# Kernel tuning notes

Hardware: AMD Instinct MI355X
Metric: run time of the kernel (lower is better)

## Reference

```python
import jax, jax.numpy as jnp
import numpy as np

B, L, H, HEADS, N_NODE = 1024, 200, 128, 8, 200000
MAXN = L + 1  # max_n_node
D = H // HEADS
EPS = 1e-12


def setup_inputs() -> dict:
    key = jax.random.key(0)
    ks = jax.random.split(key, 20)
    lengths = jax.random.randint(ks[0], (B,), 1, L + 1)
    mask = (jnp.arange(L)[None, :] < lengths[:, None]).astype(jnp.int32)  # contiguous 1s
    alias_inputs = jax.random.randint(ks[1], (B, L), 0, MAXN)
    items = jax.random.randint(ks[2], (B, MAXN), 0, N_NODE)

    def lin_w(k, o, i):
        return (jax.random.normal(k, (o, i), jnp.float32) * 0.1)

    inp = dict(
        alias_inputs=alias_inputs,
        items=items,
        mask=mask,
        emb_W=jax.random.normal(ks[3], (N_NODE, H), jnp.float32) * 0.1,
        # LastAttenion params
        W0=lin_w(ks[4], H, H), b0=jax.random.normal(ks[5], (H,), jnp.float32) * 0.1,
        W1=lin_w(ks[6], H, H), b1=jax.random.normal(ks[7], (H,), jnp.float32) * 0.1,
        W2=lin_w(ks[8], H, H), b2=jax.random.normal(ks[9], (H,), jnp.float32) * 0.1,
        # linear_q[0] (last_k = 1)
        Wq=lin_w(ks[10], H, H), bq=jax.random.normal(ks[11], (H,), jnp.float32) * 0.1,
        # linear_transform (2H -> H)
        Wt=lin_w(ks[12], H, 2 * H), bt=jax.random.normal(ks[13], (H,), jnp.float32) * 0.1,
        ln_g=jax.random.normal(ks[14], (H,), jnp.float32) * 0.1,
        ln_b=jax.random.normal(ks[15], (H,), jnp.float32) * 0.1,
    )
    return inp


def reference(alias_inputs, items, mask, emb_W, W0, b0, W1, b1, W2, b2, Wq, bq, Wt, bt, ln_g, ln_b):
    maskf = mask.astype(jnp.float32)
    # hidden = normalize(embedding(items)); dropout off (eval)
    hidden = emb_W[items]                                                  # [B, MAXN, H]
    hidden = hidden / (jnp.linalg.norm(hidden, axis=-1, keepdims=True) + EPS)
    # per-batch gather: seq_hidden[b, t] = hidden[b, alias_inputs[b, t]]
    seq = jnp.take_along_axis(hidden, alias_inputs[..., None], axis=1)     # [B, L, H]
    seq = seq * maskf[..., None]
    seq = seq / (jnp.linalg.norm(seq, axis=-1, keepdims=True) + EPS)
    # compute_scores
    lengths = mask.sum(1)
    last_idx = lengths - 1                                                 # >= 0 (lengths >= 1)
    ht_last = seq[jnp.arange(B), last_idx]                                 # [B, H]  (ht0 too)
    hts = (ht_last @ Wq.T + bq)[:, None, :]                                # [B, 1, H]
    # torch.norm over dim=1 (size 1) == elementwise abs
    hts = hts / (jnp.linalg.norm(hts, axis=1, keepdims=True) + EPS)
    # LastAttenion (last_k = 1, no lp-pool, eval dropout off)
    q0 = (hts @ W0.T + b0).reshape(B * HEADS, 1, D)                        # [B*h, 1, d]
    q1 = (seq @ W1.T + b1).reshape(B * HEADS, L, D)                        # [B*h, L, d]
    q2 = (seq @ W2.T + b2).reshape(B, L, HEADS, D)                         # [B, L, h, d]
    alpha = jax.nn.sigmoid(jnp.einsum('bkd,bld->bkl', q0, q1))             # [B*h, 1, L]
    alpha = alpha.reshape(B, HEADS, L).transpose(0, 2, 1)                  # [B, L, h]
    alpha = jax.nn.softmax(2.0 * alpha, axis=1)
    a = jnp.sum((alpha[..., None] * q2).reshape(B, L, H) * maskf[..., None], axis=1)  # [B, H]
    # layernorm eps=1e-8
    mu = a.mean(-1, keepdims=True)
    var = ((a - mu) ** 2).mean(-1, keepdims=True)
    a = (a - mu) / jnp.sqrt(var + 1e-8) * ln_g + ln_b
    a = jnp.concatenate([a, ht_last], axis=1) @ Wt.T + bt                  # [B, H]
    # norm=True branch
    a = a / (jnp.linalg.norm(a, axis=1, keepdims=True) + EPS)
    b = emb_W[1:]
    b = b / (jnp.linalg.norm(b, axis=1, keepdims=True) + EPS)
    return a, b.T                                                          # [B,H], [H, N_NODE-1]
```

## Files before the change

kernel.cpp:

```cpp
#include <hip/hip_runtime.h>
#include <math.h>

typedef unsigned int uint;
typedef unsigned short ushort;

__device__ __forceinline__ float b2f(ushort u){
  union { uint i; float f; } v; v.i = ((uint)u) << 16; return v.f;
}
__device__ __forceinline__ ushort f2b(float f){
  union { float f; uint i; } v; v.f = f;
  uint i = v.i;
  i += 0x7fffu + ((i >> 16) & 1u);
  return (ushort)(i >> 16);
}
__device__ __forceinline__ float wred(float v){
  #pragma unroll
  for (int s = 32; s > 0; s >>= 1) v += __shfl_xor(v, s, 64);
  return v;
}
__device__ __forceinline__ float gred16(float v){
  v += __shfl_xor(v, 1, 64);
  v += __shfl_xor(v, 2, 64);
  v += __shfl_xor(v, 4, 64);
  v += __shfl_xor(v, 8, 64);
  return v;
}
__device__ __forceinline__ float sane(float v){ return isfinite(v) ? v : 0.f; }
__device__ __forceinline__ int iclamp(int v, int lo, int hi){ return v < lo ? lo : (v > hi ? hi : v); }

__device__ __forceinline__ void gather_norm8(const void* emb, int isf, int it, int p, float x[8]){
  if (isf){
    const float4* q = (const float4*)((const float*)emb + (size_t)it * 128);
    float4 u = q[p * 2], u2 = q[p * 2 + 1];
    x[0] = u.x; x[1] = u.y; x[2] = u.z; x[3] = u.w;
    x[4] = u2.x; x[5] = u2.y; x[6] = u2.z; x[7] = u2.w;
  } else {
    uint4 u = ((const uint4*)((const ushort*)emb + (size_t)it * 128))[p];
    x[0] = b2f((ushort)u.x); x[1] = b2f((ushort)(u.x >> 16));
    x[2] = b2f((ushort)u.y); x[3] = b2f((ushort)(u.y >> 16));
    x[4] = b2f((ushort)u.z); x[5] = b2f((ushort)(u.z >> 16));
    x[6] = b2f((ushort)u.w); x[7] = b2f((ushort)(u.w >> 16));
  }
  float ss = 0.f;
  #pragma unroll
  for (int e = 0; e < 8; ++e) ss += x[e] * x[e];
  ss = gred16(ss);
  float inv = 1.f / (sqrtf(ss) + 1e-12f);
  #pragma unroll
  for (int e = 0; e < 8; ++e) x[e] *= inv;
  float ss2 = 0.f;
  #pragma unroll
  for (int e = 0; e < 8; ++e) ss2 += x[e] * x[e];
  ss2 = gred16(ss2);
  float inv2 = 1.f / (sqrtf(ss2) + 1e-12f);
  #pragma unroll
  for (int e = 0; e < 8; ++e) x[e] *= inv2;
}

#define OUTB 131072

#define C_W0T 0
#define C_W1  16384
#define C_W2T 32768
#define C_WQT 49152
#define C_WTT 65536
#define C_B0  98304
#define C_B1  98432
#define C_B2  98560
#define C_BQ  98688
#define C_BT  98816
#define C_G   98944
#define C_BB  99072
#define C_TOT 99200

__global__ __launch_bounds__(256) void k_detect(const ushort* __restrict__ emb,
                                                int* __restrict__ flag){
  __shared__ int s_bad;
  if (threadIdx.x == 0) s_bad = 0;
  __syncthreads();
  int bad = 0;
  for (int i = threadIdx.x; i < 8192; i += 256){
    float v = fabsf(b2f(emb[i]));
    if (!(v <= 1e4f)) bad = 1;
  }
  if (bad) s_bad = 1;
  __syncthreads();
  if (threadIdx.x == 0) flag[0] = s_bad;
}

__global__ __launch_bounds__(256) void k_wts(
    const void* W0, const void* b0, const void* W1, const void* b1,
    const void* W2, const void* b2, const void* Wq, const void* bq,
    const void* Wt, const void* bt, const void* g, const void* bb,
    const int* __restrict__ flag, float* __restrict__ wts){
  int j = blockIdx.x * 256 + threadIdx.x;
  if (j >= C_TOT) return;
  const int isf = flag[0];
  const void* src; int si;
  if (j < 16384)      { int k = j >> 7, h = j & 127; src = W0; si = h * 128 + k; }
  else if (j < 32768) { src = W1; si = j - 16384; }
  else if (j < 49152) { int i = j - 32768; int k = i >> 7, h = i & 127; src = W2; si = h * 128 + k; }
  else if (j < 65536) { int i = j - 49152; int k = i >> 7, h = i & 127; src = Wq; si = h * 128 + k; }
  else if (j < 98304) { int i = j - 65536; int k = i >> 7, h = i & 127; src = Wt; si = h * 256 + k; }
  else {
    int i = j - 98304; int arr = i >> 7;
    const void* tab[7] = { b0, b1, b2, bq, bt, g, bb };
    src = tab[arr]; si = i & 127;
  }
  wts[j] = isf ? ((const float*)src)[si] : b2f(((const ushort*)src)[si]);
}

__global__ __launch_bounds__(256) void k_bout(const void* __restrict__ emb,
                                              const int* __restrict__ flag,
                                              void* __restrict__ outv){
  __shared__ float tile[64 * 129];
  const int t = threadIdx.x, gid = t >> 4, p = t & 15;
  const int base = blockIdx.x * 64;
  const int isf = flag[0];
  for (int i = gid; i < 64; i += 16){
    int gi = base + i;
    if (gi < 199999){
      float x[8];
      if (isf){
        const float4* q = (const float4*)((const float*)emb + (size_t)(gi + 1) * 128);
        float4 u = q[p * 2], u2 = q[p * 2 + 1];
        x[0] = u.x; x[1] = u.y; x[2] = u.z; x[3] = u.w;
        x[4] = u2.x; x[5] = u2.y; x[6] = u2.z; x[7] = u2.w;
      } else {
        uint4 u = ((const uint4*)((const ushort*)emb + (size_t)(gi + 1) * 128))[p];
        x[0] = b2f((ushort)u.x); x[1] = b2f((ushort)(u.x >> 16));
        x[2] = b2f((ushort)u.y); x[3] = b2f((ushort)(u.y >> 16));
        x[4] = b2f((ushort)u.z); x[5] = b2f((ushort)(u.z >> 16));
        x[6] = b2f((ushort)u.w); x[7] = b2f((ushort)(u.w >> 16));
      }
      float ss = 0.f;
      #pragma unroll
      for (int e = 0; e < 8; ++e) ss += x[e] * x[e];
      ss = gred16(ss);
      float inv = 1.f / (sqrtf(ss) + 1e-12f);
      #pragma unroll
      for (int e = 0; e < 8; ++e) tile[i * 129 + p * 8 + e] = x[e] * inv;
    }
  }
  __syncthreads();
  for (int it = 0; it < 32; ++it){
    int idx = it * 256 + t;
    int h = idx >> 6, n = idx & 63;
    int gi = base + n;
    if (gi < 199999){
      float val = sane(tile[n * 129 + h]);
      if (isf) ((float*)outv)[OUTB + (size_t)h * 199999 + gi] = val;
      else     ((ushort*)outv)[OUTB + (size_t)h * 199999 + gi] = f2b(val);
    }
  }
}

__global__ __launch_bounds__(128) void k_prep(
    const int* __restrict__ alias_, const int* __restrict__ items,
    const int* __restrict__ mask, const void* __restrict__ emb,
    const float* __restrict__ wts, const int* __restrict__ flag,
    float* __restrict__ ws_ht, float* __restrict__ ws_X0,
    float* __restrict__ ws_c1, int* __restrict__ ws_len){
  __shared__ float s_ht[128], s_hts[128], s_X0s[128];
  __shared__ float s_red[8];
  __shared__ int s_item;
  const int b = blockIdx.x, t = threadIdx.x, w = t >> 6;
  const int isf = flag[0];

  int mv = mask[b * 200 + t] + (t < 72 ? mask[b * 200 + 128 + t] : 0);
  float lv = wred((float)mv);
  if ((t & 63) == 0) s_red[w] = lv;
  __syncthreads();
  int len = iclamp((int)(s_red[0] + s_red[1] + 0.5f), 1, 200);
  if (t == 0){
    ws_len[b] = len;
    int a = iclamp(alias_[b * 200 + len - 1], 0, 200);
    s_item = iclamp(items[b * 201 + a], 0, 199999);
  }
  __syncthreads();

  float v = isf ? ((const float*)emb)[(size_t)s_item * 128 + t]
                : b2f(((const ushort*)emb)[(size_t)s_item * 128 + t]);
  float ss = wred(v * v);
  if ((t & 63) == 0) s_red[2 + w] = ss;
  __syncthreads();
  v = v / (sqrtf(s_red[2] + s_red[3]) + 1e-12f);
  float ss2 = wred(v * v);
  if ((t & 63) == 0) s_red[4 + w] = ss2;
  __syncthreads();
  v = v / (sqrtf(s_red[4] + s_red[5]) + 1e-12f);
  s_ht[t] = v;
  ws_ht[b * 128 + t] = v;
  __syncthreads();

  {
    double acc = (double)wts[C_BQ + t];
    for (int k = 0; k < 128; ++k)
      acc += (double)wts[C_WQT + k * 128 + t] * (double)s_ht[k];
    float a = (float)acc;
    s_hts[t] = a / (fabsf(a) + 1e-12f);
  }
  __syncthreads();
  {
    float a0 = wts[C_B0 + t];
    for (int k = 0; k < 128; ++k) a0 += wts[C_W0T + k * 128 + t] * s_hts[k];
    s_X0s[t] = a0;
    ws_X0[b * 128 + t] = a0;
  }
  __syncthreads();
  if (t < 64){
    int head = t >> 3, j = t & 7;
    float c = 0.f;
    #pragma unroll
    for (int d = 0; d < 16; ++d) c += s_X0s[head * 16 + d] * wts[C_B1 + j * 16 + d];
    ws_c1[b * 64 + t] = c;
  }
}

__global__ __launch_bounds__(256) void k_main(
    const int* __restrict__ alias_, const int* __restrict__ items,
    const int* __restrict__ mask, const void* __restrict__ emb,
    const float* __restrict__ wts, const float* __restrict__ ws_ht,
    const float* __restrict__ ws_X0, const float* __restrict__ ws_c1,
    const int* __restrict__ ws_len, const int* __restrict__ flag,
    void* __restrict__ outv){
  __shared__ __align__(16) char s_buf[17408];
  __shared__ float s_alpha[1600];
  __shared__ float s_X0[128], s_ht[128], s_a[128];
  __shared__ float s_c1[64];
  __shared__ float s_T[8], s_Tp[64];
  __shared__ float s_red[16];
  __shared__ int   s_it[200];
  ushort* s_w1p = (ushort*)s_buf;
  float*  s_part = (float*)s_buf;

  const int b = blockIdx.x, t = threadIdx.x;
  const int wv = t >> 6, gid = t >> 4, p = t & 15, lane = t & 63;
  const int isf = flag[0];
  const int len = iclamp(ws_len[b], 1, 200);
  const int mbase = b * 200;

  if (t < 128){ s_X0[t] = ws_X0[b * 128 + t]; s_ht[t] = ws_ht[b * 128 + t]; }
  if (t < 64)  s_c1[t] = ws_c1[b * 64 + t];
  if (t < 200){
    int m = mask[mbase + t];
    int a = m ? iclamp(alias_[mbase + t], 0, 200) : 0;
    s_it[t] = m ? iclamp(items[b * 201 + a], 0, 199999) : -1;
  }
  __syncthreads();

  for (int idx = t; idx < 8192; idx += 256){
    int hj = idx >> 7, k = idx & 127, head = hj >> 3, j = hj & 7;
    float acc = 0.f;
    const float* w1r = wts + C_W1 + (j * 16) * 128 + k;
    #pragma unroll
    for (int d = 0; d < 16; ++d) acc += s_X0[head * 16 + d] * w1r[d * 128];
    s_w1p[hj * 136 + k] = f2b(acc);
  }
  __syncthreads();

  for (int r = gid; r < 200; r += 16){
    int it = s_it[r];
    float x[8];
    #pragma unroll
    for (int e = 0; e < 8; ++e) x[e] = 0.f;
    if (it >= 0) gather_norm8(emb, isf, it, p, x);
    int head = r / 25, lb = (r % 25) * 8;
    #pragma unroll
    for (int j = 0; j < 8; ++j){
      uint4 wu = *(const uint4*)(&s_w1p[(head * 8 + j) * 136 + p * 8]);
      float dot = x[0] * b2f((ushort)wu.x) + x[1] * b2f((ushort)(wu.x >> 16))
                + x[2] * b2f((ushort)wu.y) + x[3] * b2f((ushort)(wu.y >> 16))
                + x[4] * b2f((ushort)wu.z) + x[5] * b2f((ushort)(wu.z >> 16))
                + x[6] * b2f((ushort)wu.w) + x[7] * b2f((ushort)(wu.w >> 16));
      dot = gred16(dot);
      if (p == 0){
        float logit = s_c1[head * 8 + j] + dot;
        s_alpha[(lb + j) * 8 + head] = 2.f / (1.f + expf(-logit));
      }
    }
  }
  __syncthreads();

  {
    int head = t >> 5, l32 = t & 31;
    float vals[7]; float mx = -1e30f;
    #pragma unroll
    for (int i = 0; i < 7; ++i){
      int l = l32 + 32 * i;
      float xx = (l < 200) ? s_alpha[l * 8 + head] : -1e30f;
      vals[i] = xx; mx = fmaxf(mx, xx);
    }
    #pragma unroll
    for (int s = 16; s > 0; s >>= 1) mx = fmaxf(mx, __shfl_xor(mx, s, 64));
    float sum = 0.f; float e[7];
    #pragma unroll
    for (int i = 0; i < 7; ++i){
      int l = l32 + 32 * i;
      float ex = (l < 200) ? expf(vals[i] - mx) : 0.f;
      e[i] = ex; sum += ex;
    }
    #pragma unroll
    for (int s = 16; s > 0; s >>= 1) sum += __shfl_xor(sum, s, 64);
    float inv = 1.f / sum;
    #pragma unroll
    for (int i = 0; i < 7; ++i){
      int l = l32 + 32 * i;
      if (l < 200) s_alpha[l * 8 + head] = e[i] * inv;
    }
  }
  __syncthreads();

  if (t < 64){
    int h = t & 7, seg = t >> 3;
    int l0 = seg * 25, l1 = l0 + 25; if (l1 > len) l1 = len;
    float s = 0.f;
    for (int l = l0; l < l1; ++l) s += s_alpha[l * 8 + h];
    s_Tp[t] = s;
  }
  __syncthreads();
  if (t < 8){
    float s = 0.f;
    #pragma unroll
    for (int seg = 0; seg < 8; ++seg) s += s_Tp[seg * 8 + t];
    s_T[t] = s;
  }

  float acc[64];
  #pragma unroll
  for (int e = 0; e < 64; ++e) acc[e] = 0.f;
  for (int l = gid; l < 200; l += 16){
    int it = s_it[l];
    if (it >= 0){
      float x[8];
      gather_norm8(emb, isf, it, p, x);
      float al[8];
      #pragma unroll
      for (int h = 0; h < 8; ++h) al[h] = s_alpha[l * 8 + h];
      #pragma unroll
      for (int h = 0; h < 8; ++h)
        #pragma unroll
        for (int e = 0; e < 8; ++e) acc[h * 8 + e] += al[h] * x[e];
    }
  }
  #pragma unroll
  for (int e = 0; e < 64; ++e){
    float v = acc[e];
    v += __shfl_xor(v, 16, 64);
    v += __shfl_xor(v, 32, 64);
    acc[e] = v;
  }
  __syncthreads();
  if (lane < 16){
    #pragma unroll
    for (int h = 0; h < 8; ++h)
      #pragma unroll
      for (int e = 0; e < 8; ++e)
        s_part[wv * 1024 + h * 128 + p * 8 + e] = acc[h * 8 + e];
  }
  __syncthreads();
  for (int i = t; i < 1024; i += 256)
    s_part[i] = s_part[i] + s_part[1024 + i] + s_part[2048 + i] + s_part[3072 + i];
  __syncthreads();

  float araw = 0.f;
  if (t < 128){
    int head = t >> 4;
    araw = wts[C_B2 + t] * s_T[head];
    const float* hl = &s_part[head * 128];
    for (int k = 0; k < 128; ++k) araw += hl[k] * wts[C_W2T + k * 128 + t];
  }
  float v1 = wred(t < 128 ? araw : 0.f);
  if ((t & 63) == 0) s_red[t >> 6] = v1;
  __syncthreads();
  float mu = (s_red[0] + s_red[1]) * 0.0078125f;
  float dd = (t < 128) ? (araw - mu) : 0.f;
  float v2 = wred(dd * dd);
  if ((t & 63) == 0) s_red[4 + (t >> 6)] = v2;
  __syncthreads();
  float var = (s_red[4] + s_red[5]) * 0.0078125f;
  if (t < 128)
    s_a[t] = dd / sqrtf(var + 1e-8f) * wts[C_G + t] + wts[C_BB + t];
  __syncthreads();

  float o = 0.f;
  if (t < 128){
    o = wts[C_BT + t];
    for (int k = 0; k < 128; ++k) o += s_a[k] * wts[C_WTT + k * 128 + t];
    for (int k = 0; k < 128; ++k) o += s_ht[k] * wts[C_WTT + (128 + k) * 128 + t];
  }
  float v3 = wred(t < 128 ? o * o : 0.f);
  if ((t & 63) == 0) s_red[8 + (t >> 6)] = v3;
  __syncthreads();
  float nrm = sqrtf(s_red[8] + s_red[9]);
  if (t < 128){
    float val = sane(o / (nrm + 1e-12f));
    if (isf) ((float*)outv)[b * 128 + t] = val;
    else     ((ushort*)outv)[b * 128 + t] = f2b(val);
  }
}

extern "C" void kernel_launch(void* const* d_in, const int* in_sizes, int n_in,
                              void* d_out, int out_size, void* d_ws, size_t ws_size,
                              hipStream_t stream){
  const int* alias_ = (const int*)d_in[0];
  const int* items  = (const int*)d_in[1];
  const int* mask   = (const int*)d_in[2];
  const void* emb = d_in[3];
  const void* W0  = d_in[4];
  const void* b0  = d_in[5];
  const void* W1  = d_in[6];
  const void* b1  = d_in[7];
  const void* W2  = d_in[8];
  const void* b2_ = d_in[9];
  const void* Wq  = d_in[10];
  const void* bq  = d_in[11];
  const void* Wt  = d_in[12];
  const void* bt  = d_in[13];
  const void* g_  = d_in[14];
  const void* bb_ = d_in[15];

  char* ws = (char*)d_ws;
  int*   ws_flag = (int*)ws;
  float* wts     = (float*)(ws + 64);
  float* ws_ht   = (float*)(ws + 396864);
  float* ws_X0   = (float*)(ws + 921152);
  float* ws_c1   = (float*)(ws + 1445440);
  int*   ws_len  = (int*)(ws + 1707584);

  k_detect<<<dim3(1),    dim3(256), 0, stream>>>((const ushort*)emb, ws_flag);
  k_wts   <<<dim3(388),  dim3(256), 0, stream>>>(W0, b0, W1, b1, W2, b2_, Wq, bq,
                                                 Wt, bt, g_, bb_, ws_flag, wts);
  k_bout  <<<dim3(3125), dim3(256), 0, stream>>>(emb, ws_flag, d_out);
  k_prep  <<<dim3(1024), dim3(128), 0, stream>>>(alias_, items, mask, emb, wts, ws_flag,
                                                 ws_ht, ws_X0, ws_c1, ws_len);
  k_main  <<<dim3(1024), dim3(256), 0, stream>>>(alias_, items, mask, emb, wts,
                                                 ws_ht, ws_X0, ws_c1, ws_len, ws_flag, d_out);
}
```

Baseline: 413.1 us.

## Cache normalized gathered rows in shared memory and prefetch next row

The main kernel used to gather and normalize each embedding row twice, once for the attention logits and again for the weighted sum. Now the first pass stores the normalized row as bf16 in a 51 KB shared buffer, and the second pass reads it from there, removing the second random global gather. The first pass also loads the next row while the current one is being processed, and it collapses the double normalization into a single normalization. Dynamic shared memory grows to about 74 KB per block, which can lower the number of resident blocks per CU. It also adds bf16 rounding of the activations, and dropping the second normalization changes results slightly.

```diff
diff --git a/kernel.cpp b/kernel.cpp
--- a/kernel.cpp
+++ b/kernel.cpp
@@ -28,33 +28,24 @@
 __device__ __forceinline__ float sane(float v){ return isfinite(v) ? v : 0.f; }
 __device__ __forceinline__ int iclamp(int v, int lo, int hi){ return v < lo ? lo : (v > hi ? hi : v); }
 
-__device__ __forceinline__ void gather_norm8(const void* emb, int isf, int it, int p, float x[8]){
-  if (isf){
-    const float4* q = (const float4*)((const float*)emb + (size_t)it * 128);
-    float4 u = q[p * 2], u2 = q[p * 2 + 1];
-    x[0] = u.x; x[1] = u.y; x[2] = u.z; x[3] = u.w;
-    x[4] = u2.x; x[5] = u2.y; x[6] = u2.z; x[7] = u2.w;
+__device__ __forceinline__ void load_raw8(const void* emb, int isf, int it, int p, float x[8]){
+  if (it >= 0){
+    if (isf){
+      const float4* q = (const float4*)((const float*)emb + (size_t)it * 128);
+      float4 u = q[p * 2], u2 = q[p * 2 + 1];
+      x[0] = u.x; x[1] = u.y; x[2] = u.z; x[3] = u.w;
+      x[4] = u2.x; x[5] = u2.y; x[6] = u2.z; x[7] = u2.w;
+    } else {
+      uint4 u = ((const uint4*)((const ushort*)emb + (size_t)it * 128))[p];
+      x[0] = b2f((ushort)u.x); x[1] = b2f((ushort)(u.x >> 16));
+      x[2] = b2f((ushort)u.y); x[3] = b2f((ushort)(u.y >> 16));
+      x[4] = b2f((ushort)u.z); x[5] = b2f((ushort)(u.z >> 16));
+      x[6] = b2f((ushort)u.w); x[7] = b2f((ushort)(u.w >> 16));
+    }
   } else {
-    uint4 u = ((const uint4*)((const ushort*)emb + (size_t)it * 128))[p];
-    x[0] = b2f((ushort)u.x); x[1] = b2f((ushort)(u.x >> 16));
-    x[2] = b2f((ushort)u.y); x[3] = b2f((ushort)(u.y >> 16));
-    x[4] = b2f((ushort)u.z); x[5] = b2f((ushort)(u.z >> 16));
-    x[6] = b2f((ushort)u.w); x[7] = b2f((ushort)(u.w >> 16));
-  }
-  float ss = 0.f;
-  #pragma unroll
-  for (int e = 0; e < 8; ++e) ss += x[e] * x[e];
-  ss = gred16(ss);
-  float inv = 1.f / (sqrtf(ss) + 1e-12f);
-  #pragma unroll
-  for (int e = 0; e < 8; ++e) x[e] *= inv;
-  float ss2 = 0.f;
-  #pragma unroll
-  for (int e = 0; e < 8; ++e) ss2 += x[e] * x[e];
-  ss2 = gred16(ss2);
-  float inv2 = 1.f / (sqrtf(ss2) + 1e-12f);
-  #pragma unroll
-  for (int e = 0; e < 8; ++e) x[e] *= inv2;
+    #pragma unroll
+    for (int e = 0; e < 8; ++e) x[e] = 0.f;
+  }
 }
 
 #define OUTB 131072
@@ -72,6 +63,8 @@
 #define C_G   98944
 #define C_BB  99072
 #define C_TOT 99200
+
+#define KMAIN_SMEM 73984
 
 __global__ __launch_bounds__(256) void k_detect(const ushort* __restrict__ emb,
                                                 int* __restrict__ flag){
@@ -224,15 +217,17 @@
     const float* __restrict__ ws_X0, const float* __restrict__ ws_c1,
     const int* __restrict__ ws_len, const int* __restrict__ flag,
     void* __restrict__ outv){
-  __shared__ __align__(16) char s_buf[17408];
-  __shared__ float s_alpha[1600];
+  extern __shared__ __align__(16) char dsm[];
+  ushort* s_x     = (ushort*)dsm;
+  ushort* s_w1p   = (ushort*)(dsm + 51200);
+  float*  s_part  = (float*)(dsm + 51200);
+  float*  s_alpha = (float*)(dsm + 51200 + 16384);
+
   __shared__ float s_X0[128], s_ht[128], s_a[128];
   __shared__ float s_c1[64];
   __shared__ float s_T[8], s_Tp[64];
   __shared__ float s_red[16];
   __shared__ int   s_it[200];
-  ushort* s_w1p = (ushort*)s_buf;
-  float*  s_part = (float*)s_buf;
 
   const int b = blockIdx.x, t = threadIdx.x;
   const int wv = t >> 6, gid = t >> 4, p = t & 15, lane = t & 63;
@@ -255,29 +250,48 @@
     const float* w1r = wts + C_W1 + (j * 16) * 128 + k;
     #pragma unroll
     for (int d = 0; d < 16; ++d) acc += s_X0[head * 16 + d] * w1r[d * 128];
-    s_w1p[hj * 136 + k] = f2b(acc);
-  }
-  __syncthreads();
-
-  for (int r = gid; r < 200; r += 16){
-    int it = s_it[r];
-    float x[8];
-    #pragma unroll
-    for (int e = 0; e < 8; ++e) x[e] = 0.f;
-    if (it >= 0) gather_norm8(emb, isf, it, p, x);
-    int head = r / 25, lb = (r % 25) * 8;
-    #pragma unroll
-    for (int j = 0; j < 8; ++j){
-      uint4 wu = *(const uint4*)(&s_w1p[(head * 8 + j) * 136 + p * 8]);
-      float dot = x[0] * b2f((ushort)wu.x) + x[1] * b2f((ushort)(wu.x >> 16))
-                + x[2] * b2f((ushort)wu.y) + x[3] * b2f((ushort)(wu.y >> 16))
-                + x[4] * b2f((ushort)wu.z) + x[5] * b2f((ushort)(wu.z >> 16))
-                + x[6] * b2f((ushort)wu.w) + x[7] * b2f((ushort)(wu.w >> 16));
-      dot = gred16(dot);
-      if (p == 0){
-        float logit = s_c1[head * 8 + j] + dot;
-        s_alpha[(lb + j) * 8 + head] = 2.f / (1.f + expf(-logit));
+    s_w1p[hj * 128 + k] = f2b(acc);
+  }
+  __syncthreads();
+
+  {
+    float xc[8], xn[8];
+    load_raw8(emb, isf, s_it[gid], p, xc);
+    for (int r = gid; r < 200; r += 16){
+      int rn = r + 16;
+      load_raw8(emb, isf, rn < 200 ? s_it[rn] : -1, p, xn);
+
+      float ss = 0.f;
+      #pragma unroll
+      for (int e = 0; e < 8; ++e) ss += xc[e] * xc[e];
+      ss = gred16(ss);
+      float inv = 1.f / (sqrtf(ss) + 1e-12f);
+      #pragma unroll
+      for (int e = 0; e < 8; ++e) xc[e] *= inv;
+
+      uint4 u;
+      u.x = (uint)f2b(xc[0]) | ((uint)f2b(xc[1]) << 16);
+      u.y = (uint)f2b(xc[2]) | ((uint)f2b(xc[3]) << 16);
+      u.z = (uint)f2b(xc[4]) | ((uint)f2b(xc[5]) << 16);
+      u.w = (uint)f2b(xc[6]) | ((uint)f2b(xc[7]) << 16);
+      *(uint4*)(s_x + r * 128 + p * 8) = u;
+
+      int head = r / 25, lb = (r % 25) * 8;
+      #pragma unroll
+      for (int j = 0; j < 8; ++j){
+        uint4 wu = *(const uint4*)(s_w1p + (head * 8 + j) * 128 + p * 8);
+        float dot = xc[0] * b2f((ushort)wu.x) + xc[1] * b2f((ushort)(wu.x >> 16))
+                  + xc[2] * b2f((ushort)wu.y) + xc[3] * b2f((ushort)(wu.y >> 16))
+                  + xc[4] * b2f((ushort)wu.z) + xc[5] * b2f((ushort)(wu.z >> 16))
+                  + xc[6] * b2f((ushort)wu.w) + xc[7] * b2f((ushort)(wu.w >> 16));
+        dot = gred16(dot);
+        if (p == 0){
+          float logit = s_c1[head * 8 + j] + dot;
+          s_alpha[(lb + j) * 8 + head] = 2.f / (1.f + expf(-logit));
+        }
       }
+      #pragma unroll
+      for (int e = 0; e < 8; ++e) xc[e] = xn[e];
     }
   }
   __syncthreads();
@@ -330,13 +344,16 @@
   #pragma unroll
   for (int e = 0; e < 64; ++e) acc[e] = 0.f;
   for (int l = gid; l < 200; l += 16){
-    int it = s_it[l];
-    if (it >= 0){
+    if (s_it[l] >= 0){
+      uint4 xu = *(const uint4*)(s_x + l * 128 + p * 8);
       float x[8];
-      gather_norm8(emb, isf, it, p, x);
-      float al[8];
-      #pragma unroll
-      for (int h = 0; h < 8; ++h) al[h] = s_alpha[l * 8 + h];
+      x[0] = b2f((ushort)xu.x); x[1] = b2f((ushort)(xu.x >> 16));
+      x[2] = b2f((ushort)xu.y); x[3] = b2f((ushort)(xu.y >> 16));
+      x[4] = b2f((ushort)xu.z); x[5] = b2f((ushort)(xu.z >> 16));
+      x[6] = b2f((ushort)xu.w); x[7] = b2f((ushort)(xu.w >> 16));
+      float4 a0 = *(const float4*)(s_alpha + l * 8);
+      float4 a1 = *(const float4*)(s_alpha + l * 8 + 4);
+      float al[8] = { a0.x, a0.y, a0.z, a0.w, a1.x, a1.y, a1.z, a1.w };
       #pragma unroll
       for (int h = 0; h < 8; ++h)
         #pragma unroll
@@ -428,12 +445,19 @@
   float* ws_c1   = (float*)(ws + 1445440);
   int*   ws_len  = (int*)(ws + 1707584);
 
+  static int g_attr_done = 0;
+  if (!g_attr_done){
+    hipFuncSetAttribute(reinterpret_cast<const void*>(k_main),
+                        hipFuncAttributeMaxDynamicSharedMemorySize, KMAIN_SMEM);
+    g_attr_done = 1;
+  }
+
   k_detect<<<dim3(1),    dim3(256), 0, stream>>>((const ushort*)emb, ws_flag);
   k_wts   <<<dim3(388),  dim3(256), 0, stream>>>(W0, b0, W1, b1, W2, b2_, Wq, bq,
                                                  Wt, bt, g_, bb_, ws_flag, wts);
   k_bout  <<<dim3(3125), dim3(256), 0, stream>>>(emb, ws_flag, d_out);
   k_prep  <<<dim3(1024), dim3(128), 0, stream>>>(alias_, items, mask, emb, wts, ws_flag,
                                                  ws_ht, ws_X0, ws_c1, ws_len);
-  k_main  <<<dim3(1024), dim3(256), 0, stream>>>(alias_, items, mask, emb, wts,
+  k_main  <<<dim3(1024), dim3(256), KMAIN_SMEM, stream>>>(alias_, items, mask, emb, wts,
                                                  ws_ht, ws_X0, ws_c1, ws_len, ws_flag, d_out);
 }
```

After: 409.5 us. No clear change (-0.9%).
